# Kernel optimization log

Measured on AMD Instinct MI355X. Metric: run time of the kernel, lower is better.

Reference implementation:

```python
import jax, jax.numpy as jnp
import numpy as np

CONT_FIELD = 13
CATE_FIELD = 26
VOCAB = 100000
EMB_DIM = 40
ATTN_DIM = 8
BATCH = 4096


def setup_inputs() -> dict:
    key = jax.random.key(0)
    ks = jax.random.split(key, 8)
    conts = jax.random.uniform(ks[0], (BATCH, CONT_FIELD), dtype=jnp.float32)
    cates = jax.random.randint(ks[1], (BATCH, CATE_FIELD), 0, VOCAB, dtype=jnp.int64)
    combs = jax.random.normal(ks[2], (BATCH, 1), dtype=jnp.float32)
    a = np.square(3.0 / (CATE_FIELD * EMB_DIM))
    emb_table = jax.random.uniform(ks[3], (VOCAB, EMB_DIM), minval=-a, maxval=a, dtype=jnp.float32)
    attn_W = jax.random.normal(ks[4], (ATTN_DIM, EMB_DIM), dtype=jnp.float32) * 0.1
    attn_b = jnp.zeros((ATTN_DIM,), dtype=jnp.float32)
    proj_W = jax.random.normal(ks[5], (1, ATTN_DIM), dtype=jnp.float32) * 0.3
    fc_W = jax.random.normal(ks[6], (1, EMB_DIM), dtype=jnp.float32) * 0.1
    fc_b = jnp.zeros((1,), dtype=jnp.float32)
    return {"conts": conts, "cates": cates, "combs": combs, "emb_table": emb_table,
            "attn_W": attn_W, "attn_b": attn_b, "proj_W": proj_W, "fc_W": fc_W, "fc_b": fc_b}


def reference(conts, cates, combs, emb_table, attn_W, attn_b, proj_W, fc_W, fc_b):
    # continuous fields use fixed embedding rows 0..CONT_FIELD-1 scaled by value
    cont_emb = emb_table[jnp.arange(CONT_FIELD)][None, :, :] * conts[:, :, None]  # (B, 13, D)
    cate_emb = emb_table[cates]                                                   # (B, 26, D)
    x = jnp.concatenate([cont_emb, cate_emb], axis=1)                             # (B, 39, D)
    row, col = jnp.triu_indices(CONT_FIELD + CATE_FIELD, k=1)                     # 741 pairs
    ewp = x[:, row, :] * x[:, col, :]                                             # (B, 741, D)
    h = jax.nn.relu(jnp.einsum('bpd,ad->bpa', ewp, attn_W) + attn_b)              # (B, 741, 8)
    logits = jnp.einsum('bpa,oa->bpo', h, proj_W)                                 # (B, 741, 1)
    attn = jax.nn.softmax(logits, axis=1)                                         # softmax over pairs
    pooled = jnp.sum(attn * ewp, axis=1)                                          # (B, D)
    out = jax.nn.sigmoid(pooled @ fc_W.T + fc_b)                                  # (B, 1)
    return out
```

## Files before the change

kernel.cpp:

```cpp
#include <hip/hip_runtime.h>
#include <math.h>

#define NF 39
#define CONT_F 13
#define CATE_F 26
#define EMB_D 40
#define VOCAB 100000
#define NCH 9

typedef __attribute__((ext_vector_type(8))) short short8;
typedef __attribute__((ext_vector_type(4))) float f32x4;

union frag { short8 s; uint4 u; };

__device__ __forceinline__ unsigned pk2(float a, float b) {
    return __builtin_amdgcn_perm(__float_as_uint(b), __float_as_uint(a), 0x07060302u);
}

__global__ __launch_bounds__(256, 2)
void afm_wave_kernel(const float* __restrict__ conts,
                     const int*   __restrict__ cates,
                     const float* __restrict__ emb,
                     const float* __restrict__ attn_W,
                     const float* __restrict__ attn_b,
                     const float* __restrict__ proj_W,
                     const float* __restrict__ fc_W,
                     const float* __restrict__ fc_b,
                     float* __restrict__ out,
                     int batch)
{
    __shared__ __attribute__((aligned(16))) float Wlds[NCH * EMB_D];

    const int tid = threadIdx.x;
    if (tid < NCH * 10) {
        const int c = tid / 10, q = tid % 10;
        ((float4*)Wlds)[tid] = (c < 8) ? ((const float4*)attn_W)[c * 10 + q]
                                       : ((const float4*)fc_W)[q];
    }

    float pj[8], bb[8];
    #pragma unroll
    for (int a = 0; a < 8; ++a) { pj[a] = proj_W[a]; bb[a] = attn_b[a]; }
    const float fcb = fc_b[0];

    __syncthreads();

    const int wave = tid >> 6;
    const int lane = tid & 63;
    const int l15  = lane & 15;
    const int quad = lane >> 4;
    const int row  = blockIdx.x * 4 + wave;
    if (row >= batch) return;

    int erow[3];
    float cs = 1.f;
    const bool contl = (l15 < CONT_F);
    if (contl) {
        erow[0] = l15;
        cs = conts[row * CONT_F + l15];
    } else {
        unsigned u = (unsigned)cates[row * CATE_F + (l15 - CONT_F)];
        erow[0] = (u >= (unsigned)VOCAB) ? 0 : (int)u;
    }
    {
        unsigned u = (unsigned)cates[row * CATE_F + (3 + l15)];
        erow[1] = (u >= (unsigned)VOCAB) ? 0 : (int)u;
    }
    {
        int f2 = 32 + l15; if (f2 > NF - 1) f2 = NF - 1;
        unsigned u = (unsigned)cates[row * CATE_F + (f2 - CONT_F)];
        erow[2] = (u >= (unsigned)VOCAB) ? 0 : (int)u;
    }

    float xf[3][8];
    float xe[3][2];
    #pragma unroll
    for (int m = 0; m < 3; ++m) {
        const char* rp = (const char*)emb + (size_t)erow[m] * 160;
        const float4 h0 = *(const float4*)(rp + quad * 32);
        const float4 h1 = *(const float4*)(rp + quad * 32 + 16);
        const float2 t0 = *(const float2*)(rp + 128 + quad * 8);
        xf[m][0] = h0.x; xf[m][1] = h0.y; xf[m][2] = h0.z; xf[m][3] = h0.w;
        xf[m][4] = h1.x; xf[m][5] = h1.y; xf[m][6] = h1.z; xf[m][7] = h1.w;
        xe[m][0] = t0.x; xe[m][1] = t0.y;
    }
    if (contl) {
        #pragma unroll
        for (int t = 0; t < 8; ++t) xf[0][t] *= cs;
        xe[0][0] *= cs; xe[0][1] *= cs;
    }

    frag xb[3], xb2[3];
    const unsigned onew = (quad == 0) ? pk2(1.0f, 0.0f) : 0u;
    #pragma unroll
    for (int m = 0; m < 3; ++m) {
        xb[m].u = make_uint4(pk2(xf[m][0], xf[m][1]), pk2(xf[m][2], xf[m][3]),
                             pk2(xf[m][4], xf[m][5]), pk2(xf[m][6], xf[m][7]));
        xb2[m].u = make_uint4(pk2(xe[m][0], xe[m][1]), onew, 0u, 0u);
    }

    static const int TM[6] = {0, 0, 0, 1, 1, 2};
    static const int TN[6] = {0, 1, 2, 1, 2, 2};
    float lacc[6][4] = {{0.f}};
    float gv[6][4];

    #pragma unroll
    for (int c = 0; c < NCH; ++c) {
        const float* wrow = Wlds + c * EMB_D;
        const float4 w0 = *(const float4*)(wrow + quad * 8);
        const float4 w1 = *(const float4*)(wrow + quad * 8 + 4);
        const float2 wt = *(const float2*)(wrow + 32 + quad * 2);
        const unsigned bw = (quad == 0 && c < 8) ? pk2(bb[c], 0.0f) : 0u;

        frag a0[3], a1[3];
        #pragma unroll
        for (int m = 0; m < 3; ++m) {
            a0[m].u = make_uint4(pk2(xf[m][0] * w0.x, xf[m][1] * w0.y),
                                 pk2(xf[m][2] * w0.z, xf[m][3] * w0.w),
                                 pk2(xf[m][4] * w1.x, xf[m][5] * w1.y),
                                 pk2(xf[m][6] * w1.z, xf[m][7] * w1.w));
            a1[m].u = make_uint4(pk2(xe[m][0] * wt.x, xe[m][1] * wt.y), bw, 0u, 0u);
        }

        #pragma unroll
        for (int tt = 0; tt < 6; ++tt) {
            f32x4 t = {0.f, 0.f, 0.f, 0.f};
            t = __builtin_amdgcn_mfma_f32_16x16x32_bf16(a0[TM[tt]].s, xb[TN[tt]].s, t, 0, 0, 0);
            t = __builtin_amdgcn_mfma_f32_16x16x32_bf16(a1[TM[tt]].s, xb2[TN[tt]].s, t, 0, 0, 0);
            if (c < 8) {
                #pragma unroll
                for (int rr = 0; rr < 4; ++rr)
                    lacc[tt][rr] = fmaf(pj[c], fmaxf(t[rr], 0.f), lacc[tt][rr]);
            } else {
                #pragma unroll
                for (int rr = 0; rr < 4; ++rr) gv[tt][rr] = t[rr];
            }
        }
    }

    float s = 0.f, gs = 0.f;
    #pragma unroll
    for (int tt = 0; tt < 6; ++tt) {
        #pragma unroll
        for (int rr = 0; rr < 4; ++rr) {
            const int i = TM[tt] * 16 + quad * 4 + rr;
            const int j = TN[tt] * 16 + l15;
            if (i < j && j < NF) {
                const float e = __expf(lacc[tt][rr]);
                s += e;
                gs = fmaf(e, gv[tt][rr], gs);
            }
        }
    }
    #pragma unroll
    for (int off = 32; off; off >>= 1) {
        s  += __shfl_xor(s, off);
        gs += __shfl_xor(gs, off);
    }
    if (lane == 0) {
        const float zf = gs / s + fcb;
        out[row] = 1.f / (1.f + __expf(-zf));
    }
}

extern "C" void kernel_launch(void* const* d_in, const int* in_sizes, int n_in,
                              void* d_out, int out_size, void* d_ws, size_t ws_size,
                              hipStream_t stream) {
    const float* conts  = (const float*)d_in[0];
    const int*   cates  = (const int*)  d_in[1];
    const float* emb    = (const float*)d_in[3];
    const float* attn_W = (const float*)d_in[4];
    const float* attn_b = (const float*)d_in[5];
    const float* proj_W = (const float*)d_in[6];
    const float* fc_W   = (const float*)d_in[7];
    const float* fc_b   = (const float*)d_in[8];
    float* out = (float*)d_out;

    const int batch = in_sizes[0] / CONT_F;
    const int grid = (batch + 3) / 4;
    afm_wave_kernel<<<grid, 256, 0, stream>>>(
        conts, cates, emb, attn_W, attn_b, proj_W, fc_W, fc_b, out, batch);
}
```

Baseline: 91.56 us.

## Keep embeddings bf16-packed in registers and raise occupancy to four blocks

Embedding values are stored only as packed bf16 words instead of fp32 arrays, unpacked on the fly with shifts and masks when forming the weighted A operands. The fc gate values are also stored as packed bf16. Launch bounds are raised from 2 to 4 blocks per CU. Together these cut register pressure so more waves can hide gather latency, at the cost of extra unpack ALU work per chunk and slightly lower precision in the products and gate values.

```diff
diff --git a/kernel.cpp b/kernel.cpp
--- a/kernel.cpp
+++ b/kernel.cpp
@@ -16,8 +16,10 @@
 __device__ __forceinline__ unsigned pk2(float a, float b) {
     return __builtin_amdgcn_perm(__float_as_uint(b), __float_as_uint(a), 0x07060302u);
 }
+__device__ __forceinline__ float lo16(unsigned w) { return __uint_as_float(w << 16); }
+__device__ __forceinline__ float hi16(unsigned w) { return __uint_as_float(w & 0xFFFF0000u); }
 
-__global__ __launch_bounds__(256, 2)
+__global__ __launch_bounds__(256, 4)
 void afm_wave_kernel(const float* __restrict__ conts,
                      const int*   __restrict__ cates,
                      const float* __restrict__ emb,
@@ -72,37 +74,29 @@
         erow[2] = (u >= (unsigned)VOCAB) ? 0 : (int)u;
     }
 
-    float xf[3][8];
-    float xe[3][2];
+    frag xb[3];
+    unsigned xw2[3];
     #pragma unroll
     for (int m = 0; m < 3; ++m) {
         const char* rp = (const char*)emb + (size_t)erow[m] * 160;
-        const float4 h0 = *(const float4*)(rp + quad * 32);
-        const float4 h1 = *(const float4*)(rp + quad * 32 + 16);
-        const float2 t0 = *(const float2*)(rp + 128 + quad * 8);
-        xf[m][0] = h0.x; xf[m][1] = h0.y; xf[m][2] = h0.z; xf[m][3] = h0.w;
-        xf[m][4] = h1.x; xf[m][5] = h1.y; xf[m][6] = h1.z; xf[m][7] = h1.w;
-        xe[m][0] = t0.x; xe[m][1] = t0.y;
+        float4 h0 = *(const float4*)(rp + quad * 32);
+        float4 h1 = *(const float4*)(rp + quad * 32 + 16);
+        float2 t0 = *(const float2*)(rp + 128 + quad * 8);
+        if (m == 0 && contl) {
+            h0.x *= cs; h0.y *= cs; h0.z *= cs; h0.w *= cs;
+            h1.x *= cs; h1.y *= cs; h1.z *= cs; h1.w *= cs;
+            t0.x *= cs; t0.y *= cs;
+        }
+        xb[m].u = make_uint4(pk2(h0.x, h0.y), pk2(h0.z, h0.w),
+                             pk2(h1.x, h1.y), pk2(h1.z, h1.w));
+        xw2[m] = pk2(t0.x, t0.y);
     }
-    if (contl) {
-        #pragma unroll
-        for (int t = 0; t < 8; ++t) xf[0][t] *= cs;
-        xe[0][0] *= cs; xe[0][1] *= cs;
-    }
-
-    frag xb[3], xb2[3];
     const unsigned onew = (quad == 0) ? pk2(1.0f, 0.0f) : 0u;
-    #pragma unroll
-    for (int m = 0; m < 3; ++m) {
-        xb[m].u = make_uint4(pk2(xf[m][0], xf[m][1]), pk2(xf[m][2], xf[m][3]),
-                             pk2(xf[m][4], xf[m][5]), pk2(xf[m][6], xf[m][7]));
-        xb2[m].u = make_uint4(pk2(xe[m][0], xe[m][1]), onew, 0u, 0u);
-    }
 
     static const int TM[6] = {0, 0, 0, 1, 1, 2};
     static const int TN[6] = {0, 1, 2, 1, 2, 2};
-    float lacc[6][4] = {{0.f}};
-    float gv[6][4];
+    float    lacc[6][4] = {{0.f}};
+    unsigned gvp[6][2];
 
     #pragma unroll
     for (int c = 0; c < NCH; ++c) {
@@ -112,28 +106,33 @@
         const float2 wt = *(const float2*)(wrow + 32 + quad * 2);
         const unsigned bw = (quad == 0 && c < 8) ? pk2(bb[c], 0.0f) : 0u;
 
-        frag a0[3], a1[3];
+        frag a0[3];
+        unsigned a1w[3];
         #pragma unroll
         for (int m = 0; m < 3; ++m) {
-            a0[m].u = make_uint4(pk2(xf[m][0] * w0.x, xf[m][1] * w0.y),
-                                 pk2(xf[m][2] * w0.z, xf[m][3] * w0.w),
-                                 pk2(xf[m][4] * w1.x, xf[m][5] * w1.y),
-                                 pk2(xf[m][6] * w1.z, xf[m][7] * w1.w));
-            a1[m].u = make_uint4(pk2(xe[m][0] * wt.x, xe[m][1] * wt.y), bw, 0u, 0u);
+            a0[m].u = make_uint4(
+                pk2(lo16(xb[m].u.x) * w0.x, hi16(xb[m].u.x) * w0.y),
+                pk2(lo16(xb[m].u.y) * w0.z, hi16(xb[m].u.y) * w0.w),
+                pk2(lo16(xb[m].u.z) * w1.x, hi16(xb[m].u.z) * w1.y),
+                pk2(lo16(xb[m].u.w) * w1.z, hi16(xb[m].u.w) * w1.w));
+            a1w[m] = pk2(lo16(xw2[m]) * wt.x, hi16(xw2[m]) * wt.y);
         }
 
         #pragma unroll
         for (int tt = 0; tt < 6; ++tt) {
+            frag A2, B2;
+            A2.u = make_uint4(a1w[TM[tt]], bw,   0u, 0u);
+            B2.u = make_uint4(xw2[TN[tt]], onew, 0u, 0u);
             f32x4 t = {0.f, 0.f, 0.f, 0.f};
             t = __builtin_amdgcn_mfma_f32_16x16x32_bf16(a0[TM[tt]].s, xb[TN[tt]].s, t, 0, 0, 0);
-            t = __builtin_amdgcn_mfma_f32_16x16x32_bf16(a1[TM[tt]].s, xb2[TN[tt]].s, t, 0, 0, 0);
+            t = __builtin_amdgcn_mfma_f32_16x16x32_bf16(A2.s, B2.s, t, 0, 0, 0);
             if (c < 8) {
                 #pragma unroll
                 for (int rr = 0; rr < 4; ++rr)
                     lacc[tt][rr] = fmaf(pj[c], fmaxf(t[rr], 0.f), lacc[tt][rr]);
             } else {
-                #pragma unroll
-                for (int rr = 0; rr < 4; ++rr) gv[tt][rr] = t[rr];
+                gvp[tt][0] = pk2(t[0], t[1]);
+                gvp[tt][1] = pk2(t[2], t[3]);
             }
         }
     }
@@ -141,6 +140,9 @@
     float s = 0.f, gs = 0.f;
     #pragma unroll
     for (int tt = 0; tt < 6; ++tt) {
+        const float g0 = lo16(gvp[tt][0]), g1 = hi16(gvp[tt][0]);
+        const float g2 = lo16(gvp[tt][1]), g3 = hi16(gvp[tt][1]);
+        const float gq[4] = {g0, g1, g2, g3};
         #pragma unroll
         for (int rr = 0; rr < 4; ++rr) {
             const int i = TM[tt] * 16 + quad * 4 + rr;
@@ -148,7 +150,7 @@
             if (i < j && j < NF) {
                 const float e = __expf(lacc[tt][rr]);
                 s += e;
-                gs = fmaf(e, gv[tt][rr], gs);
+                gs = fmaf(e, gq[rr], gs);
             }
         }
     }
```

Measured after the change: 149.2 us. +63.0%, slower.
